# Kernel tuning notes

Measured on AMD Instinct MI355X. Metric: run time of the kernel, lower is better.

The kernel has to match this reference:

```python
import jax, jax.numpy as jnp
import numpy as np

B, S, DM, H = 8, 512, 1024, 16
D = DM // H            # head_dim = 64
NFEAT = 4              # len(feature_types)
N_DIST = 2 * 512 - 1   # max_utt_num*2-1 = 1023
N_DISC = 16 + 1        # len(DISCOURSE_RELATIONS)+1
N_COOC = 5 + 1


def setup_inputs() -> dict:
    key = jax.random.key(0)
    ks = jax.random.split(key, 24)
    inp = {}
    inp["query"] = jax.random.normal(ks[0], (B, S, DM), jnp.float32)
    inp["key"] = jax.random.normal(ks[1], (B, S, DM), jnp.float32)
    inp["value"] = jax.random.normal(ks[2], (B, S, DM), jnp.float32)
    inp["distance_adj"] = jax.random.randint(ks[3], (B, S, S), 0, N_DIST).astype(jnp.int32)
    inp["speaker_adj"] = jax.random.uniform(ks[4], (B, S, S), jnp.float32)
    inp["discourse_adj"] = jax.random.randint(ks[5], (B, S, S), 0, N_DISC).astype(jnp.int32)
    inp["cooccurrence_adj"] = jax.random.randint(ks[6], (B, S, S), 0, N_COOC).astype(jnp.int32)
    inp["mask"] = jnp.ones((B, 1, 1, S), jnp.int32)
    w = lambda k, shape: jax.random.normal(k, shape, jnp.float32) * 0.02
    inp["Wq"] = w(ks[7], (DM, DM)); inp["bq"] = jnp.zeros((DM,), jnp.float32)
    inp["Wk"] = w(ks[8], (DM, DM)); inp["bk"] = jnp.zeros((DM,), jnp.float32)
    inp["Wv"] = w(ks[9], (DM, DM)); inp["bv"] = jnp.zeros((DM,), jnp.float32)
    inp["Wo"] = w(ks[10], (DM, DM)); inp["bo"] = jnp.zeros((DM,), jnp.float32)
    inp["dist_embed"] = w(ks[11], (N_DIST, 1))
    inp["disc_embed"] = w(ks[12], (N_DISC, 1)).at[0].set(0.0)  # padding_idx=0
    inp["cooc_embed"] = w(ks[13], (N_COOC, 1)).at[0].set(0.0)  # padding_idx=0
    inp["fcw"] = w(ks[14], (H, NFEAT))       # per-head 1x1 conv weights
    inp["fcb"] = jnp.zeros((H,), jnp.float32)
    inp["cw"] = w(ks[15], (2,))              # combine conv weights
    inp["cb"] = jnp.zeros((), jnp.float32)
    return inp


def reference(query, key, value, distance_adj, speaker_adj, discourse_adj,
              cooccurrence_adj, mask, Wq, bq, Wk, bk, Wv, bv, Wo, bo,
              dist_embed, disc_embed, cooc_embed, fcw, fcb, cw, cb):
    scale = jnp.asarray(D ** 0.5, query.dtype)
    # Linear projections, split heads -> [B, H, S, D]
    split = lambda x: x.reshape(B, S, H, D).transpose(0, 2, 1, 3)
    Q = split(query @ Wq.T + bq)
    K = split(key @ Wk.T + bk)
    V = split(value @ Wv.T + bv)
    energy = jnp.einsum('bhqd,bhkd->bhqk', Q, K) / scale  # [B,H,S,S]
    # Adjacency feature maps in feature_types order: distance, speaker, discourse, cooccurrence
    dist = dist_embed[distance_adj, 0]
    disc = disc_embed[discourse_adj, 0] * (discourse_adj != 0)
    cooc = cooc_embed[cooccurrence_adj, 0] * (cooccurrence_adj != 0)
    feature_map = jnp.stack([dist, speaker_adj, disc, cooc], axis=1)  # [B,4,S,S]
    # Per-head 1x1 conv over the 4 feature channels + relu
    feat = jax.nn.relu(jnp.einsum('hc,bcij->bhij', fcw, feature_map)
                       + fcb[None, :, None, None])       # [B,H,S,S]
    # Combine conv (1x1, 2 channels -> 1) + relu
    energy = jax.nn.relu(cw[0] * energy + cw[1] * feat + cb)
    energy = jnp.where(mask == 0, -jnp.inf, energy)
    attention = jax.nn.softmax(energy, axis=-1)           # [B,H,S,S]
    x = jnp.einsum('bhqk,bhkd->bhqd', attention, V)       # dropout p=0 (eval)
    x = x.transpose(0, 2, 1, 3).reshape(B, S, DM)
    x = x @ Wo.T + bo
    return x, attention
```

## Files before the change

kernel.cpp:

```cpp
#include <hip/hip_runtime.h>

using short8 = __attribute__((ext_vector_type(8))) short;
using f32x4  = __attribute__((ext_vector_type(4))) float;
typedef unsigned short u16x4 __attribute__((ext_vector_type(4)));

__device__ __forceinline__ unsigned short f2bf(float x) {
    union { float f; unsigned u; } v; v.f = x;
    unsigned u = v.u;
    unsigned r = (u + 0x7fffu + ((u >> 16) & 1u)) >> 16;
    return (unsigned short)r;
}
__device__ __forceinline__ float bf2f(unsigned short h) {
    union { unsigned u; float f; } v; v.u = ((unsigned)h) << 16;
    return v.f;
}

__device__ __forceinline__ void async16(const void* g, void* l) {
    __builtin_amdgcn_global_load_lds(
        (const __attribute__((address_space(1))) void*)g,
        (__attribute__((address_space(3))) void*)l, 16, 0, 0);
}

__device__ __forceinline__ short8 lds_swz8(const unsigned short* base, int row,
                                           int colbyte, int stride) {
    const char* p = (const char*)base + row * stride + (colbyte ^ ((row & 7) << 4));
    return *(const short8*)p;
}

__global__ __launch_bounds__(256) void cvt_all(
    const float* __restrict__ q, const float* __restrict__ k, const float* __restrict__ v,
    const float* __restrict__ wq, const float* __restrict__ wk,
    const float* __restrict__ wv, const float* __restrict__ wo,
    unsigned short* __restrict__ dstA, unsigned short* __restrict__ dstW)
{
    int bx = blockIdx.x;
    const float* src;
    unsigned short* o;
    size_t i;
    if (bx < 6144) {
        int z = bx >> 11;
        src = (z == 0) ? q : ((z == 1) ? k : v);
        o = dstA + (size_t)z * 4194304;
        i = ((size_t)(bx & 2047) * 256 + threadIdx.x) * 8;
    } else {
        int z = (bx - 6144) >> 9;
        src = (z == 0) ? wq : ((z == 1) ? wk : ((z == 2) ? wv : wo));
        o = dstW + (size_t)z * 1048576;
        i = ((size_t)((bx - 6144) & 511) * 256 + threadIdx.x) * 8;
    }
    float4 a = *(const float4*)(src + i);
    float4 b = *(const float4*)(src + i + 4);
    ushort4 lo, hi;
    lo.x = f2bf(a.x); lo.y = f2bf(a.y); lo.z = f2bf(a.z); lo.w = f2bf(a.w);
    hi.x = f2bf(b.x); hi.y = f2bf(b.y); hi.z = f2bf(b.z); hi.w = f2bf(b.w);
    *(ushort4*)(o + i) = lo;
    *(ushort4*)(o + i + 4) = hi;
}

__global__ __launch_bounds__(256) void feat_kernel(
    const int* __restrict__ dist_adj, const float* __restrict__ spk,
    const int* __restrict__ disc_adj, const int* __restrict__ cooc_adj,
    const float* __restrict__ dist_emb, const float* __restrict__ disc_emb,
    const float* __restrict__ cooc_emb, const float* __restrict__ fcw,
    const float* __restrict__ fcb, const float* __restrict__ cw,
    unsigned short* __restrict__ G)
{
    __shared__ float s_dist[1023];
    __shared__ float s_disc[17];
    __shared__ float s_cooc[6];
    __shared__ float s_fcw[64];
    __shared__ float s_fcb[16];
    int tid = threadIdx.x;
    for (int i = tid; i < 1023; i += 256) s_dist[i] = dist_emb[i];
    if (tid < 17) s_disc[tid] = disc_emb[tid];
    if (tid < 6)  s_cooc[tid] = cooc_emb[tid];
    if (tid < 64) s_fcw[tid]  = fcw[tid];
    if (tid < 16) s_fcb[tid]  = fcb[tid];
    __syncthreads();
    float cw1 = cw[1];

    int bx = blockIdx.x;
    int k  = (bx & 1) * 256 + tid;
    int qq = (bx >> 1) & 127;
    int b  = bx >> 8;

    size_t abase = ((size_t)b * 512 + qq * 4) * 512 + k;
    float f0[4], f1[4], f2[4], f3[4];
#pragma unroll
    for (int r = 0; r < 4; ++r) {
        size_t a = abase + (size_t)r * 512;
        int dd = __builtin_nontemporal_load(dist_adj + a);
        f1[r]  = __builtin_nontemporal_load(spk + a);
        int dc = __builtin_nontemporal_load(disc_adj + a);
        int cc = __builtin_nontemporal_load(cooc_adj + a);
        f0[r] = s_dist[dd];
        f2[r] = dc ? s_disc[dc] : 0.f;
        f3[r] = cc ? s_cooc[cc] : 0.f;
    }

    size_t gq = ((size_t)b * 16 * 128 + qq) * 512 + k;
#pragma unroll
    for (int h = 0; h < 16; ++h) {
        float w0 = s_fcw[h*4+0], w1 = s_fcw[h*4+1], w2 = s_fcw[h*4+2], w3 = s_fcw[h*4+3];
        float bb = s_fcb[h];
        u16x4 o;
        o[0] = f2bf(fmaxf(w0*f0[0] + w1*f1[0] + w2*f2[0] + w3*f3[0] + bb, 0.f) * cw1);
        o[1] = f2bf(fmaxf(w0*f0[1] + w1*f1[1] + w2*f2[1] + w3*f3[1] + bb, 0.f) * cw1);
        o[2] = f2bf(fmaxf(w0*f0[2] + w1*f1[2] + w2*f2[2] + w3*f3[2] + bb, 0.f) * cw1);
        o[3] = f2bf(fmaxf(w0*f0[3] + w1*f1[3] + w2*f2[3] + w3*f3[3] + bb, 0.f) * cw1);
        __builtin_nontemporal_store(o, (u16x4*)(G + (gq + (size_t)h * 65536) * 4));
    }
}

template<int OMODE>
__device__ __forceinline__ void gemm_bf16_body(
    const unsigned short* __restrict__ A, const unsigned short* __restrict__ W,
    const float* __restrict__ bias, void* __restrict__ outp, int m0, int n0)
{
    __shared__ __align__(16) unsigned short As[128 * 32];
    __shared__ __align__(16) unsigned short Bs[128 * 32];
    int tid = threadIdx.x;
    int lane = tid & 63, wid = tid >> 6;
    int wx = wid & 1, wy = wid >> 1;
    int lanelo = lane & 15, hi8 = (lane >> 4) * 8;
    int rowc = lane >> 2;
    int colc = (lane & 3) * 8;

    f32x4 acc[4][4];
#pragma unroll
    for (int i = 0; i < 4; ++i)
#pragma unroll
        for (int j = 0; j < 4; ++j) {
            acc[i][j][0] = 0.f; acc[i][j][1] = 0.f; acc[i][j][2] = 0.f; acc[i][j][3] = 0.f;
        }

    for (int kk = 0; kk < 32; ++kk) {
        int k0 = kk * 32;
        __syncthreads();
#pragma unroll
        for (int p = 0; p < 2; ++p) {
            int c = 2 * wid + p;
            int row = c * 16 + rowc;
            async16(A + (size_t)(m0 + row) * 1024 + k0 + colc, As + c * 512);
        }
#pragma unroll
        for (int p = 0; p < 2; ++p) {
            int c = 2 * wid + p;
            int row = c * 16 + rowc;
            async16(W + (size_t)(n0 + row) * 1024 + k0 + colc, Bs + c * 512);
        }
        __syncthreads();

        short8 af[4], bfr[4];
#pragma unroll
        for (int i = 0; i < 4; ++i)
            af[i] = *(const short8*)(As + (wy*64 + i*16 + lanelo) * 32 + hi8);
#pragma unroll
        for (int j = 0; j < 4; ++j)
            bfr[j] = *(const short8*)(Bs + (wx*64 + j*16 + lanelo) * 32 + hi8);
#pragma unroll
        for (int i = 0; i < 4; ++i)
#pragma unroll
            for (int j = 0; j < 4; ++j)
                acc[i][j] = __builtin_amdgcn_mfma_f32_16x16x32_bf16(af[i], bfr[j], acc[i][j], 0, 0, 0);
    }

    float bia[4];
#pragma unroll
    for (int j = 0; j < 4; ++j) bia[j] = bias[n0 + wx*64 + j*16 + lanelo];
#pragma unroll
    for (int i = 0; i < 4; ++i) {
        int mbase = m0 + wy*64 + i*16 + (lane >> 4) * 4;
#pragma unroll
        for (int j = 0; j < 4; ++j) {
            int n = n0 + wx*64 + j*16 + lanelo;
            if (OMODE == 2) {
                ushort4 o4;
                o4.x = f2bf(acc[i][j][0] + bia[j]);
                o4.y = f2bf(acc[i][j][1] + bia[j]);
                o4.z = f2bf(acc[i][j][2] + bia[j]);
                o4.w = f2bf(acc[i][j][3] + bia[j]);
                unsigned short* o = (unsigned short*)outp;
                size_t addr = ((size_t)((mbase >> 9) * 16 + (n >> 6)) * 64 + (n & 63)) * 512
                              + (mbase & 511);
                *(ushort4*)(o + addr) = o4;
            } else {
#pragma unroll
                for (int r = 0; r < 4; ++r) {
                    int m = mbase + r;
                    float val = acc[i][j][r] + bia[j];
                    if (OMODE == 0) {
                        unsigned short* o = (unsigned short*)outp;
                        o[((size_t)((m >> 9) * 16 + (n >> 6)) * 512 + (m & 511)) * 64 + (n & 63)] = f2bf(val);
                    } else {
                        float* o = (float*)outp;
                        o[(size_t)m * 1024 + n] = val;
                    }
                }
            }
        }
    }
}

__global__ __launch_bounds__(256) void gemm_qkv(
    const unsigned short* __restrict__ Abf, const unsigned short* __restrict__ Wbf,
    const float* __restrict__ bq, const float* __restrict__ bk, const float* __restrict__ bv,
    unsigned short* Qb, unsigned short* Kb, unsigned short* Vt)
{
    int z = blockIdx.z;
    const unsigned short* A = Abf + (size_t)z * 4194304;
    const unsigned short* W = Wbf + (size_t)z * 1048576;
    if (z == 2) {
        gemm_bf16_body<2>(A, W, bv, Vt, blockIdx.x * 128, blockIdx.y * 128);
    } else {
        const float* bias = (z == 0) ? bq : bk;
        unsigned short* o = (z == 0) ? Qb : Kb;
        gemm_bf16_body<0>(A, W, bias, o, blockIdx.x * 128, blockIdx.y * 128);
    }
}

__global__ __launch_bounds__(256) void gemm_proj(
    const unsigned short* __restrict__ xh, const unsigned short* __restrict__ Wo,
    const float* __restrict__ bo, float* __restrict__ out)
{
    gemm_bf16_body<1>(xh, Wo, bo, out, blockIdx.x * 128, blockIdx.y * 128);
}

__global__ __launch_bounds__(256, 2) void attn_kernel(
    const unsigned short* __restrict__ Qb, const unsigned short* __restrict__ Kb,
    const unsigned short* __restrict__ Vt, const unsigned short* __restrict__ G,
    const int* __restrict__ mask, const float* __restrict__ cw,
    const float* __restrict__ cb, float* __restrict__ attn_out,
    unsigned short* __restrict__ xh)
{
    __shared__ __align__(16) char smem[35840];
    unsigned short* Qs = (unsigned short*)smem;
    unsigned short* Ks = (unsigned short*)(smem + 8192);
    unsigned short* Vs = (unsigned short*)smem;
    unsigned short* Ps = (unsigned short*)(smem + 16384);
    int* s_mask = (int*)(smem + 33792);

    int tid = threadIdx.x;
    int lane = tid & 63, w = tid >> 6;
    int lanelo = lane & 15, hi8 = (lane >> 4) * 8;
    int hi2 = lane >> 4;

    int lin = blockIdx.x;
    int xcd = lin & 7;
    int s   = lin >> 3;
    int bh  = xcd * 16 + (s >> 3);
    int qt  = s & 7;
    int b   = bh >> 4, h = bh & 15;

    float qs  = cw[0] * 0.125f;
    float cbv = cb[0];

    s_mask[tid]       = mask[b * 512 + tid];
    s_mask[tid + 256] = mask[b * 512 + tid + 256];

    int r8  = lane >> 3;
    int gs8 = (lane & 7) ^ r8;
#pragma unroll
    for (int p = 0; p < 2; ++p) {
        int row = p * 32 + w * 8 + r8;
        async16(Qb + ((size_t)bh * 512 + qt * 64 + row) * 64 + gs8 * 8,
                Qs + (p * 32 + w * 8) * 64);
    }
    __syncthreads();

    short8 aq[2];
    aq[0] = lds_swz8(Qs, w * 16 + lanelo, hi8 * 2, 128);
    aq[1] = lds_swz8(Qs, w * 16 + lanelo, 64 + hi8 * 2, 128);
    int qrow = qt * 64 + w * 16 + hi2 * 4;
    int qq   = qt * 16 + w * 4 + hi2;
    const unsigned short* gbase = G + ((size_t)bh * 128 + qq) * 2048;

    float P[32][4];
#pragma unroll
    for (int kt = 0; kt < 4; ++kt) {
        u16x4 g[8];
#pragma unroll
        for (int j = 0; j < 8; ++j)
            g[j] = __builtin_nontemporal_load(
                (const u16x4*)(gbase + (kt * 8 + j) * 64 + lanelo * 4));
        __syncthreads();
#pragma unroll
        for (int p = 0; p < 4; ++p) {
            int row = p * 32 + w * 8 + r8;
            async16(Kb + ((size_t)bh * 512 + kt * 128 + row) * 64 + gs8 * 8,
                    Ks + (p * 32 + w * 8) * 64);
        }
        __syncthreads();
#pragma unroll
        for (int j = 0; j < 8; ++j) {
            short8 b0 = lds_swz8(Ks, j * 16 + lanelo, hi8 * 2, 128);
            short8 b1 = lds_swz8(Ks, j * 16 + lanelo, 64 + hi8 * 2, 128);
            f32x4 acc; acc[0] = 0.f; acc[1] = 0.f; acc[2] = 0.f; acc[3] = 0.f;
            acc = __builtin_amdgcn_mfma_f32_16x16x32_bf16(aq[0], b0, acc, 0, 0, 0);
            acc = __builtin_amdgcn_mfma_f32_16x16x32_bf16(aq[1], b1, acc, 0, 0, 0);
            int jj = kt * 8 + j;
            int kcol = jj * 16 + lanelo;
            int mk = s_mask[kcol];
            float gf[4] = { bf2f((unsigned short)g[j][0]), bf2f((unsigned short)g[j][1]),
                            bf2f((unsigned short)g[j][2]), bf2f((unsigned short)g[j][3]) };
#pragma unroll
            for (int r = 0; r < 4; ++r) {
                float e = qs * acc[r] + gf[r] + cbv;
                e = fmaxf(e, 0.f);
                P[jj][r] = mk ? __expf(e) : 0.f;
            }
        }
    }

    float inv[4];
#pragma unroll
    for (int r = 0; r < 4; ++r) {
        float s0 = 0.f;
#pragma unroll
        for (int jj = 0; jj < 32; ++jj) s0 += P[jj][r];
        s0 += __shfl_xor(s0, 1, 64);
        s0 += __shfl_xor(s0, 2, 64);
        s0 += __shfl_xor(s0, 4, 64);
        s0 += __shfl_xor(s0, 8, 64);
        inv[r] = 1.0f / s0;
    }

    {
        float* ap = attn_out + ((size_t)bh * 512 + qrow) * 512 + lanelo;
#pragma unroll
        for (int jj = 0; jj < 32; ++jj)
#pragma unroll
            for (int r = 0; r < 4; ++r)
                __builtin_nontemporal_store(P[jj][r] * inv[r],
                                            ap + (size_t)r * 512 + jj * 16);
    }

    f32x4 xacc[4];
#pragma unroll
    for (int jf = 0; jf < 4; ++jf) { xacc[jf][0]=0.f; xacc[jf][1]=0.f; xacc[jf][2]=0.f; xacc[jf][3]=0.f; }

    int r8v  = ((w & 1) * 4 + hi2) & 7;
    int gs16 = (lane & 15) ^ r8v;
    unsigned short* Psw = Ps + w * 16 * 136;
#pragma unroll
    for (int c = 0; c < 4; ++c) {
        __syncthreads();
#pragma unroll
        for (int p = 0; p < 4; ++p) {
            int row = p * 16 + w * 4 + hi2;
            async16(Vt + ((size_t)bh * 64 + row) * 512 + c * 128 + gs16 * 8,
                    Vs + (p * 16 + w * 4) * 128);
        }
#pragma unroll
        for (int jc = 0; jc < 8; ++jc) {
            int jj = c * 8 + jc;
#pragma unroll
            for (int r = 0; r < 4; ++r)
                Psw[(hi2 * 4 + r) * 136 + jc * 16 + lanelo] = f2bf(P[jj][r]);
        }
        __syncthreads();
#pragma unroll
        for (int ksub = 0; ksub < 4; ++ksub) {
            short8 ap8 = *(const short8*)(Psw + (size_t)lanelo * 136 + ksub * 32 + hi8);
#pragma unroll
            for (int jf = 0; jf < 4; ++jf) {
                short8 bv = lds_swz8(Vs, jf * 16 + lanelo, ksub * 64 + hi8 * 2, 256);
                xacc[jf] = __builtin_amdgcn_mfma_f32_16x16x32_bf16(ap8, bv, xacc[jf], 0, 0, 0);
            }
        }
    }

#pragma unroll
    for (int jf = 0; jf < 4; ++jf) {
        int d = jf * 16 + lanelo;
#pragma unroll
        for (int r = 0; r < 4; ++r) {
            float val = xacc[jf][r] * inv[r];
            xh[((size_t)b * 512 + qrow + r) * 1024 + h * 64 + d] = f2bf(val);
        }
    }
}

extern "C" void kernel_launch(void* const* d_in, const int* in_sizes, int n_in,
                              void* d_out, int out_size, void* d_ws, size_t ws_size,
                              hipStream_t stream) {
    (void)in_sizes; (void)n_in; (void)out_size; (void)ws_size;
    const float* query    = (const float*)d_in[0];
    const float* key      = (const float*)d_in[1];
    const float* value    = (const float*)d_in[2];
    const int*   dist_adj = (const int*)d_in[3];
    const float* spk      = (const float*)d_in[4];
    const int*   disc_adj = (const int*)d_in[5];
    const int*   cooc_adj = (const int*)d_in[6];
    const int*   maskp    = (const int*)d_in[7];
    const float* Wq = (const float*)d_in[8];  const float* bq = (const float*)d_in[9];
    const float* Wk = (const float*)d_in[10]; const float* bk = (const float*)d_in[11];
    const float* Wv = (const float*)d_in[12]; const float* bv = (const float*)d_in[13];
    const float* Wo = (const float*)d_in[14]; const float* bo = (const float*)d_in[15];
    const float* dist_emb = (const float*)d_in[16];
    const float* disc_emb = (const float*)d_in[17];
    const float* cooc_emb = (const float*)d_in[18];
    const float* fcw = (const float*)d_in[19];
    const float* fcb = (const float*)d_in[20];
    const float* cw  = (const float*)d_in[21];
    const float* cbp = (const float*)d_in[22];

    char* w = (char*)d_ws;
    unsigned short* Qb  = (unsigned short*)(w);
    unsigned short* Kb  = (unsigned short*)(w + 8388608);
    unsigned short* Vt  = (unsigned short*)(w + 25165824);
    unsigned short* xh  = (unsigned short*)(w + 33554432);
    unsigned short* G   = (unsigned short*)(w + 41943040);
    unsigned short* Abf = G;
    unsigned short* Wbf = (unsigned short*)(w + 109051904);

    float* out_x    = (float*)d_out;
    float* attn_out = ((float*)d_out) + 4194304;

    cvt_all<<<dim3(8192, 1, 1), 256, 0, stream>>>(query, key, value, Wq, Wk, Wv, Wo,
                                                  Abf, Wbf);
    gemm_qkv<<<dim3(32, 8, 3), 256, 0, stream>>>(Abf, Wbf, bq, bk, bv, Qb, Kb, Vt);
    feat_kernel<<<2048, 256, 0, stream>>>(dist_adj, spk, disc_adj, cooc_adj,
                                          dist_emb, disc_emb, cooc_emb, fcw, fcb, cw, G);
    attn_kernel<<<dim3(1024, 1, 1), 256, 0, stream>>>(Qb, Kb, Vt, G, maskp, cw, cbp,
                                                      attn_out, xh);
    gemm_proj<<<dim3(32, 8), 256, 0, stream>>>(xh, Wbf + 3145728, bo, out_x);
}
```

Measured before the change: 385.2 us.

## Store 4 raw feature channels and apply per-head conv inside attention

The feature kernel now writes the four gathered adjacency features (bf16) per (b,q,k) instead of 16 per-head conv outputs, shrinking the intermediate buffer from B*H*S*S to B*4*S*S. The attention kernel reads those features and computes the per-head 1x1 conv, relu and cw1 scaling inline. This cuts global write and read traffic for the feature map at the cost of a few extra FMAs per score, and the same features are now reread by all 16 head blocks. Separately, the V transpose is moved out of the QKV GEMM epilogue into a dedicated LDS transpose kernel, which adds a launch and an extra pass over V.

```diff
diff --git a/kernel.cpp b/kernel.cpp
--- a/kernel.cpp
+++ b/kernel.cpp
@@ -3,6 +3,7 @@
 using short8 = __attribute__((ext_vector_type(8))) short;
 using f32x4  = __attribute__((ext_vector_type(4))) float;
 typedef unsigned short u16x4 __attribute__((ext_vector_type(4)));
+typedef unsigned short u16x8 __attribute__((ext_vector_type(8)));
 
 __device__ __forceinline__ unsigned short f2bf(float x) {
     union { float f; unsigned u; } v; v.f = x;
@@ -61,23 +62,16 @@
     const int* __restrict__ dist_adj, const float* __restrict__ spk,
     const int* __restrict__ disc_adj, const int* __restrict__ cooc_adj,
     const float* __restrict__ dist_emb, const float* __restrict__ disc_emb,
-    const float* __restrict__ cooc_emb, const float* __restrict__ fcw,
-    const float* __restrict__ fcb, const float* __restrict__ cw,
-    unsigned short* __restrict__ G)
+    const float* __restrict__ cooc_emb, unsigned short* __restrict__ F)
 {
     __shared__ float s_dist[1023];
     __shared__ float s_disc[17];
     __shared__ float s_cooc[6];
-    __shared__ float s_fcw[64];
-    __shared__ float s_fcb[16];
     int tid = threadIdx.x;
     for (int i = tid; i < 1023; i += 256) s_dist[i] = dist_emb[i];
     if (tid < 17) s_disc[tid] = disc_emb[tid];
     if (tid < 6)  s_cooc[tid] = cooc_emb[tid];
-    if (tid < 64) s_fcw[tid]  = fcw[tid];
-    if (tid < 16) s_fcb[tid]  = fcb[tid];
     __syncthreads();
-    float cw1 = cw[1];
 
     int bx = blockIdx.x;
     int k  = (bx & 1) * 256 + tid;
@@ -85,31 +79,28 @@
     int b  = bx >> 8;
 
     size_t abase = ((size_t)b * 512 + qq * 4) * 512 + k;
-    float f0[4], f1[4], f2[4], f3[4];
+    u16x8 oA, oB;
 #pragma unroll
     for (int r = 0; r < 4; ++r) {
         size_t a = abase + (size_t)r * 512;
-        int dd = __builtin_nontemporal_load(dist_adj + a);
-        f1[r]  = __builtin_nontemporal_load(spk + a);
-        int dc = __builtin_nontemporal_load(disc_adj + a);
-        int cc = __builtin_nontemporal_load(cooc_adj + a);
-        f0[r] = s_dist[dd];
-        f2[r] = dc ? s_disc[dc] : 0.f;
-        f3[r] = cc ? s_cooc[cc] : 0.f;
-    }
-
-    size_t gq = ((size_t)b * 16 * 128 + qq) * 512 + k;
-#pragma unroll
-    for (int h = 0; h < 16; ++h) {
-        float w0 = s_fcw[h*4+0], w1 = s_fcw[h*4+1], w2 = s_fcw[h*4+2], w3 = s_fcw[h*4+3];
-        float bb = s_fcb[h];
-        u16x4 o;
-        o[0] = f2bf(fmaxf(w0*f0[0] + w1*f1[0] + w2*f2[0] + w3*f3[0] + bb, 0.f) * cw1);
-        o[1] = f2bf(fmaxf(w0*f0[1] + w1*f1[1] + w2*f2[1] + w3*f3[1] + bb, 0.f) * cw1);
-        o[2] = f2bf(fmaxf(w0*f0[2] + w1*f1[2] + w2*f2[2] + w3*f3[2] + bb, 0.f) * cw1);
-        o[3] = f2bf(fmaxf(w0*f0[3] + w1*f1[3] + w2*f2[3] + w3*f3[3] + bb, 0.f) * cw1);
-        __builtin_nontemporal_store(o, (u16x4*)(G + (gq + (size_t)h * 65536) * 4));
-    }
+        int dd   = __builtin_nontemporal_load(dist_adj + a);
+        float sp = __builtin_nontemporal_load(spk + a);
+        int dc   = __builtin_nontemporal_load(disc_adj + a);
+        int cc   = __builtin_nontemporal_load(cooc_adj + a);
+        unsigned short f0 = f2bf(s_dist[dd]);
+        unsigned short f1 = f2bf(sp);
+        unsigned short f2 = f2bf(dc ? s_disc[dc] : 0.f);
+        unsigned short f3 = f2bf(cc ? s_cooc[cc] : 0.f);
+        if (r < 2) {
+            oA[r * 4 + 0] = f0; oA[r * 4 + 1] = f1; oA[r * 4 + 2] = f2; oA[r * 4 + 3] = f3;
+        } else {
+            oB[(r - 2) * 4 + 0] = f0; oB[(r - 2) * 4 + 1] = f1;
+            oB[(r - 2) * 4 + 2] = f2; oB[(r - 2) * 4 + 3] = f3;
+        }
+    }
+    unsigned short* fb = F + (((size_t)b * 128 + qq) * 512 + k) * 16;
+    *(u16x8*)(fb)     = oA;
+    *(u16x8*)(fb + 8) = oB;
 }
 
 template<int OMODE>
@@ -174,28 +165,16 @@
 #pragma unroll
         for (int j = 0; j < 4; ++j) {
             int n = n0 + wx*64 + j*16 + lanelo;
-            if (OMODE == 2) {
-                ushort4 o4;
-                o4.x = f2bf(acc[i][j][0] + bia[j]);
-                o4.y = f2bf(acc[i][j][1] + bia[j]);
-                o4.z = f2bf(acc[i][j][2] + bia[j]);
-                o4.w = f2bf(acc[i][j][3] + bia[j]);
-                unsigned short* o = (unsigned short*)outp;
-                size_t addr = ((size_t)((mbase >> 9) * 16 + (n >> 6)) * 64 + (n & 63)) * 512
-                              + (mbase & 511);
-                *(ushort4*)(o + addr) = o4;
-            } else {
-#pragma unroll
-                for (int r = 0; r < 4; ++r) {
-                    int m = mbase + r;
-                    float val = acc[i][j][r] + bia[j];
-                    if (OMODE == 0) {
-                        unsigned short* o = (unsigned short*)outp;
-                        o[((size_t)((m >> 9) * 16 + (n >> 6)) * 512 + (m & 511)) * 64 + (n & 63)] = f2bf(val);
-                    } else {
-                        float* o = (float*)outp;
-                        o[(size_t)m * 1024 + n] = val;
-                    }
+#pragma unroll
+            for (int r = 0; r < 4; ++r) {
+                int m = mbase + r;
+                float val = acc[i][j][r] + bia[j];
+                if (OMODE == 0) {
+                    unsigned short* o = (unsigned short*)outp;
+                    o[((size_t)((m >> 9) * 16 + (n >> 6)) * 512 + (m & 511)) * 64 + (n & 63)] = f2bf(val);
+                } else {
+                    float* o = (float*)outp;
+                    o[(size_t)m * 1024 + n] = val;
                 }
             }
         }
@@ -205,18 +184,14 @@
 __global__ __launch_bounds__(256) void gemm_qkv(
     const unsigned short* __restrict__ Abf, const unsigned short* __restrict__ Wbf,
     const float* __restrict__ bq, const float* __restrict__ bk, const float* __restrict__ bv,
-    unsigned short* Qb, unsigned short* Kb, unsigned short* Vt)
+    unsigned short* Qb, unsigned short* Kb, unsigned short* Vb)
 {
     int z = blockIdx.z;
     const unsigned short* A = Abf + (size_t)z * 4194304;
     const unsigned short* W = Wbf + (size_t)z * 1048576;
-    if (z == 2) {
-        gemm_bf16_body<2>(A, W, bv, Vt, blockIdx.x * 128, blockIdx.y * 128);
-    } else {
-        const float* bias = (z == 0) ? bq : bk;
-        unsigned short* o = (z == 0) ? Qb : Kb;
-        gemm_bf16_body<0>(A, W, bias, o, blockIdx.x * 128, blockIdx.y * 128);
-    }
+    const float* bias = (z == 0) ? bq : ((z == 1) ? bk : bv);
+    unsigned short* o = (z == 0) ? Qb : ((z == 1) ? Kb : Vb);
+    gemm_bf16_body<0>(A, W, bias, o, blockIdx.x * 128, blockIdx.y * 128);
 }
 
 __global__ __launch_bounds__(256) void gemm_proj(
@@ -226,11 +201,43 @@
     gemm_bf16_body<1>(xh, Wo, bo, out, blockIdx.x * 128, blockIdx.y * 128);
 }
 
+__global__ __launch_bounds__(256) void transpose_v(const unsigned short* __restrict__ Vb,
+                                                   unsigned short* __restrict__ Vt)
+{
+    __shared__ __align__(16) unsigned short T[64][72];
+    int tid = threadIdx.x;
+    int s0 = blockIdx.x * 64;
+    int bh = blockIdx.z * 16 + blockIdx.y;
+#pragma unroll
+    for (int p = 0; p < 2; ++p) {
+        int c = p * 256 + tid;
+        int row = c >> 3, kc = (c & 7) * 8;
+        uint4 v = *(const uint4*)(Vb + ((size_t)bh * 512 + s0 + row) * 64 + kc);
+        *(uint4*)&T[row][kc] = v;
+    }
+    __syncthreads();
+#pragma unroll
+    for (int p = 0; p < 2; ++p) {
+        int c = p * 256 + tid;
+        int d = c >> 3, sc = (c & 7) * 8;
+        unsigned vv[4];
+#pragma unroll
+        for (int i = 0; i < 4; ++i) {
+            unsigned lo = T[sc + 2*i][d];
+            unsigned hi = T[sc + 2*i + 1][d];
+            vv[i] = lo | (hi << 16);
+        }
+        uint4 o; o.x = vv[0]; o.y = vv[1]; o.z = vv[2]; o.w = vv[3];
+        *(uint4*)(Vt + ((size_t)bh * 64 + d) * 512 + s0 + sc) = o;
+    }
+}
+
 __global__ __launch_bounds__(256, 2) void attn_kernel(
     const unsigned short* __restrict__ Qb, const unsigned short* __restrict__ Kb,
-    const unsigned short* __restrict__ Vt, const unsigned short* __restrict__ G,
+    const unsigned short* __restrict__ Vt, const unsigned short* __restrict__ F,
     const int* __restrict__ mask, const float* __restrict__ cw,
-    const float* __restrict__ cb, float* __restrict__ attn_out,
+    const float* __restrict__ cb, const float* __restrict__ fcw,
+    const float* __restrict__ fcb, float* __restrict__ attn_out,
     unsigned short* __restrict__ xh)
 {
     __shared__ __align__(16) char smem[35840];
@@ -253,7 +260,11 @@
     int b   = bh >> 4, h = bh & 15;
 
     float qs  = cw[0] * 0.125f;
+    float cw1 = cw[1];
     float cbv = cb[0];
+    float w0 = fcw[h * 4 + 0], w1 = fcw[h * 4 + 1];
+    float w2 = fcw[h * 4 + 2], w3 = fcw[h * 4 + 3];
+    float fcb_h = fcb[h];
 
     s_mask[tid]       = mask[b * 512 + tid];
     s_mask[tid + 256] = mask[b * 512 + tid + 256];
@@ -273,16 +284,18 @@
     aq[1] = lds_swz8(Qs, w * 16 + lanelo, 64 + hi8 * 2, 128);
     int qrow = qt * 64 + w * 16 + hi2 * 4;
     int qq   = qt * 16 + w * 4 + hi2;
-    const unsigned short* gbase = G + ((size_t)bh * 128 + qq) * 2048;
+    const unsigned short* fbase = F + ((size_t)b * 128 + qq) * 512 * 16;
 
     float P[32][4];
 #pragma unroll
     for (int kt = 0; kt < 4; ++kt) {
-        u16x4 g[8];
-#pragma unroll
-        for (int j = 0; j < 8; ++j)
-            g[j] = __builtin_nontemporal_load(
-                (const u16x4*)(gbase + (kt * 8 + j) * 64 + lanelo * 4));
+        u16x8 fA[8], fB[8];
+#pragma unroll
+        for (int j = 0; j < 8; ++j) {
+            const unsigned short* fp = fbase + (size_t)((kt * 8 + j) * 16 + lanelo) * 16;
+            fA[j] = *(const u16x8*)(fp);
+            fB[j] = *(const u16x8*)(fp + 8);
+        }
         __syncthreads();
 #pragma unroll
         for (int p = 0; p < 4; ++p) {
@@ -301,11 +314,20 @@
             int jj = kt * 8 + j;
             int kcol = jj * 16 + lanelo;
             int mk = s_mask[kcol];
-            float gf[4] = { bf2f((unsigned short)g[j][0]), bf2f((unsigned short)g[j][1]),
-                            bf2f((unsigned short)g[j][2]), bf2f((unsigned short)g[j][3]) };
 #pragma unroll
             for (int r = 0; r < 4; ++r) {
-                float e = qs * acc[r] + gf[r] + cbv;
+                unsigned short e0, e1, e2, e3;
+                if (r < 2) {
+                    e0 = (unsigned short)fA[j][r*4+0]; e1 = (unsigned short)fA[j][r*4+1];
+                    e2 = (unsigned short)fA[j][r*4+2]; e3 = (unsigned short)fA[j][r*4+3];
+                } else {
+                    e0 = (unsigned short)fB[j][(r-2)*4+0]; e1 = (unsigned short)fB[j][(r-2)*4+1];
+                    e2 = (unsigned short)fB[j][(r-2)*4+2]; e3 = (unsigned short)fB[j][(r-2)*4+3];
+                }
+                float dot = w0 * bf2f(e0) + w1 * bf2f(e1) + w2 * bf2f(e2)
+                          + w3 * bf2f(e3) + fcb_h;
+                float gh = fmaxf(dot, 0.f) * cw1;
+                float e = qs * acc[r] + gh + cbv;
                 e = fmaxf(e, 0.f);
                 P[jj][r] = mk ? __expf(e) : 0.f;
             }
@@ -408,10 +430,11 @@
     char* w = (char*)d_ws;
     unsigned short* Qb  = (unsigned short*)(w);
     unsigned short* Kb  = (unsigned short*)(w + 8388608);
+    unsigned short* Vb  = (unsigned short*)(w + 16777216);
     unsigned short* Vt  = (unsigned short*)(w + 25165824);
     unsigned short* xh  = (unsigned short*)(w + 33554432);
-    unsigned short* G   = (unsigned short*)(w + 41943040);
-    unsigned short* Abf = G;
+    unsigned short* F   = (unsigned short*)(w + 41943040);
+    unsigned short* Abf = (unsigned short*)(w + 41943040);
     unsigned short* Wbf = (unsigned short*)(w + 109051904);
 
     float* out_x    = (float*)d_out;
@@ -419,10 +442,11 @@
 
     cvt_all<<<dim3(8192, 1, 1), 256, 0, stream>>>(query, key, value, Wq, Wk, Wv, Wo,
                                                   Abf, Wbf);
-    gemm_qkv<<<dim3(32, 8, 3), 256, 0, stream>>>(Abf, Wbf, bq, bk, bv, Qb, Kb, Vt);
+    gemm_qkv<<<dim3(32, 8, 3), 256, 0, stream>>>(Abf, Wbf, bq, bk, bv, Qb, Kb, Vb);
+    transpose_v<<<dim3(8, 16, 8), 256, 0, stream>>>(Vb, Vt);
     feat_kernel<<<2048, 256, 0, stream>>>(dist_adj, spk, disc_adj, cooc_adj,
-                                          dist_emb, disc_emb, cooc_emb, fcw, fcb, cw, G);
-    attn_kernel<<<dim3(1024, 1, 1), 256, 0, stream>>>(Qb, Kb, Vt, G, maskp, cw, cbp,
-                                                      attn_out, xh);
+                                          dist_emb, disc_emb, cooc_emb, F);
+    attn_kernel<<<dim3(1024, 1, 1), 256, 0, stream>>>(Qb, Kb, Vt, F, maskp, cw, cbp,
+                                                      fcw, fcb, attn_out, xh);
     gemm_proj<<<dim3(32, 8), 256, 0, stream>>>(xh, Wbf + 3145728, bo, out_x);
 }
```

Measured after the change: 410.4 us. 1.07x slower.
